# Kernel optimization log

Measured on AMD Instinct MI355X. Metric: run time of the kernel, lower is better.

## Reference

```python
import jax, jax.numpy as jnp
import numpy as np

B = 64          # batched user graphs
NPG = 512       # nodes per subgraph
N = B * NPG     # total batched nodes
DEG = 16
E = N * DEG     # edges per batched graph
DIM = 128
NUM_ENT = 1_000_000
M = 50          # candidate news entities
MASK_ID = 201659


def setup_inputs() -> dict:
    key = jax.random.key(0)
    ks = jax.random.split(key, 12)
    entity_emb = jax.random.normal(ks[0], (NUM_ENT, DIM), dtype=jnp.float32) * 0.02
    fc_w = jax.random.normal(ks[1], (DIM, DIM), dtype=jnp.float32) * 0.05
    attn_w = jax.random.normal(ks[2], (2 * DIM,), dtype=jnp.float32) * 0.05
    l_node_idx = jax.random.randint(ks[3], (N,), 0, NUM_ENT)
    s_node_idx = jax.random.randint(ks[4], (N,), 0, NUM_ENT)
    # edges confined to their own subgraph: offset by graph id
    gid = jnp.arange(E) // DEG // NPG  # [E], graph id per edge
    offs = gid * NPG
    l_src = offs + jax.random.randint(ks[5], (E,), 0, NPG)
    l_dst = offs + jax.random.randint(ks[6], (E,), 0, NPG)
    s_src = offs + jax.random.randint(ks[7], (E,), 0, NPG)
    s_dst = offs + jax.random.randint(ks[8], (E,), 0, NPG)
    goffs = jnp.arange(B) * NPG
    l_roots = goffs + jax.random.randint(ks[9], (B,), 0, NPG)
    s_roots = goffs + jax.random.randint(ks[10], (B,), 0, NPG)
    news_entities_id = jax.random.randint(ks[11], (B, M), 0, NUM_ENT)
    return {
        'entity_emb': entity_emb, 'fc_w': fc_w, 'attn_w': attn_w,
        'l_node_idx': l_node_idx, 's_node_idx': s_node_idx,
        'l_src': l_src, 'l_dst': l_dst, 's_src': s_src, 's_dst': s_dst,
        'l_roots': l_roots, 's_roots': s_roots,
        'news_entities_id': news_entities_id,
        'l_counter': 3, 's_counter': 3,
    }


def _gat(h0, src, dst, fc_w, attn_w, iters):
    """GATLayer.forward: edge attention computed once, then `iters` rounds of
    edge-softmax weighted neighbor aggregation (nodes w/o in-edges keep h)."""
    n = h0.shape[0]
    z = h0 @ fc_w  # fc (no bias)
    # e = leaky_relu(attn_fc([z_src, z_dst]))  -- [E]
    e = jax.nn.leaky_relu(z[src] @ attn_w[:DIM] + z[dst] @ attn_w[DIM:])
    # edge softmax per destination node (stable)
    m = jax.ops.segment_max(e, dst, num_segments=n)
    ex = jnp.exp(e - m[dst])
    denom = jax.ops.segment_sum(ex, dst, num_segments=n)
    alpha = ex / denom[dst]  # [E]
    has_in = jax.ops.segment_sum(jnp.ones_like(e), dst, num_segments=n) > 0
    h = z
    for _ in range(iters):
        msg = alpha[:, None] * h[src]                      # [E, DIM]
        h_new = jax.ops.segment_sum(msg, dst, num_segments=n)
        h = jnp.where(has_in[:, None], h_new, h)
    return h


def reference(entity_emb, fc_w, attn_w, l_node_idx, s_node_idx,
              l_src, l_dst, s_src, s_dst, l_roots, s_roots,
              news_entities_id, l_counter, s_counter):
    l_iters = int(l_counter) - 1
    s_iters = int(s_counter) - 1
    # long-term interest graph
    h_l = _gat(entity_emb[l_node_idx], l_src, l_dst, fc_w, attn_w, l_iters)
    l_interest = h_l[l_roots][:, None, :]   # [B,1,DIM]
    # short-term interest graph
    h_s = _gat(entity_emb[s_node_idx], s_src, s_dst, fc_w, attn_w, s_iters)
    s_interest = h_s[s_roots][:, None, :]   # [B,1,DIM]
    query = jnp.concatenate([l_interest, s_interest], axis=1)  # [B,2,DIM]
    mask = jnp.where(news_entities_id == MASK_ID, 0, news_entities_id)
    mask = mask[:, None, :].astype(jnp.float32)                # [B,1,M]
    news_emb = entity_emb[news_entities_id]                    # [B,M,DIM]
    scores = jnp.einsum('bqd,bmd->bqm', query, news_emb) / np.sqrt(DIM).astype(np.float32)
    atten = jax.nn.softmax(scores, axis=1)  # softmax over the 2 queries
    tmp = jnp.sum(scores * atten, axis=1, keepdims=True)       # [B,1,M]
    outs = jnp.sum(jnp.where(mask == 0, mask, tmp), axis=2, keepdims=True)  # [B,1,1]
    return outs
```

## Files before the change

### kernel.cpp

```cpp
#include <hip/hip_runtime.h>
#include <hip/hip_bf16.h>

#define DIM 128
#define NPG 512
#define EPG 8192
#define MAX_K 64
#define MAX_SLOTS 64
#define MASK_ID 201659

__device__ __forceinline__ float dot4(float4 a, float4 b) {
    return a.x * b.x + a.y * b.y + a.z * b.z + a.w * b.w;
}
__device__ __forceinline__ float hwred32(float p) {
    #pragma unroll
    for (int m = 16; m >= 1; m >>= 1) p += __shfl_xor(p, m);
    return p;
}
__device__ __forceinline__ float lrelu_exp(float x) {
    float lr = (x >= 0.f) ? x : 0.01f * x;
    return expf(lr);
}

__global__ __launch_bounds__(512) void k_root(
    const float* __restrict__ emb,
    const int* __restrict__ nidx_l, const int* __restrict__ nidx_s,
    const float* __restrict__ fcw, const float* __restrict__ attnw,
    const int* __restrict__ lsrc, const int* __restrict__ ldst,
    const int* __restrict__ ssrc, const int* __restrict__ sdst,
    const int* __restrict__ lroots, const int* __restrict__ sroots,
    float* __restrict__ interest)
{
    const int b = blockIdx.x, g = b >> 6, sg = b & 63, t = threadIdx.x;
    const int* src  = g ? ssrc : lsrc;
    const int* dst  = g ? sdst : ldst;
    const int* nidx = g ? nidx_s : nidx_l;
    const int root  = (g ? sroots : lroots)[sg];
    const int nbase = sg * NPG, ebase = sg * EPG;
    const int rootl = root - nbase;

    __shared__ unsigned epk[EPG];
    __shared__ float u[MAX_K][DIM];
    __shared__ short slot[MAX_K][MAX_SLOTS];
    __shared__ int   idx[NPG];
    __shared__ int   nidxs[NPG];
    __shared__ short nodeof[MAX_K];
    __shared__ int   cnt[MAX_K];
    __shared__ float wroot[MAX_SLOTS];
    __shared__ float wsrc[DIM], wdst[DIM], vvec[DIM];
    __shared__ float part[4][DIM];
    __shared__ int   Ksh;
    __shared__ float dn0sh;

    idx[t] = (t == rootl) ? 0 : -1;
    if (t < MAX_K) cnt[t] = 0;
    if (t == 0) { Ksh = 1; nodeof[0] = (short)rootl; }
    __syncthreads();

    {
        const int4* s4 = (const int4*)(src + ebase);
        const int4* d4 = (const int4*)(dst + ebase);
        #pragma unroll
        for (int i = t; i < EPG / 4; i += 512) {
            int4 s = s4[i], d = d4[i];
            unsigned p0 = ((unsigned)(s.x - nbase) << 16) | (unsigned)(d.x - nbase);
            unsigned p1 = ((unsigned)(s.y - nbase) << 16) | (unsigned)(d.y - nbase);
            unsigned p2 = ((unsigned)(s.z - nbase) << 16) | (unsigned)(d.z - nbase);
            unsigned p3 = ((unsigned)(s.w - nbase) << 16) | (unsigned)(d.w - nbase);
            ((uint4*)epk)[i] = make_uint4(p0, p1, p2, p3);
            unsigned v[4] = {p0, p1, p2, p3};
            #pragma unroll
            for (int q = 0; q < 4; q++) {
                if ((v[q] & 0xffffu) == (unsigned)rootl) {
                    int s2 = v[q] >> 16;
                    if (atomicCAS(&idx[s2], -1, -2) == -1) {
                        int k = atomicAdd(&Ksh, 1);
                        if (k < MAX_K) { nodeof[k] = (short)s2; idx[s2] = k; }
                        else idx[s2] = -1;
                    }
                }
            }
        }
        nidxs[t] = nidx[nbase + t];
        if (t < 256) {
            const float4* f4 = (const float4*)fcw;
            const float4* a4 = (const float4*)(attnw + ((t >= 128) ? DIM : 0));
            int k = t & 127;
            float s = 0.f;
            #pragma unroll 8
            for (int j = 0; j < 32; j++) s += dot4(f4[k * 32 + j], a4[j]);
            if (t < 128) wsrc[k] = s; else wdst[k] = s;
        }
    }
    __syncthreads();

    {
        const uint4* ep4 = (const uint4*)epk;
        for (int i = t; i < EPG / 4; i += 512) {
            uint4 e = ep4[i];
            unsigned v[4] = {e.x, e.y, e.z, e.w};
            #pragma unroll
            for (int q = 0; q < 4; q++) {
                int k = idx[v[q] & 0xffffu];
                if (k >= 0) {
                    int p = atomicAdd(&cnt[k], 1);
                    if (p < MAX_SLOTS) slot[k][p] = (short)(v[q] >> 16);
                }
            }
        }
    }
    __syncthreads();

    const int hwq = t >> 5, lane = t & 31;
    const int K = min(Ksh, MAX_K);
    const float4* e4 = (const float4*)emb;
    {
        float4 ws4 = ((const float4*)wsrc)[lane];
        float4 wd4 = ((const float4*)wdst)[lane];
        for (int k = hwq; k < K; k += 16) {
            int c = min(cnt[k], MAX_SLOTS);
            float4 rd = e4[(size_t)nidxs[nodeof[k]] * 32 + lane];
            float ad = hwred32(dot4(rd, wd4));
            float4 acc = make_float4(0.f, 0.f, 0.f, 0.f);
            float dn = 0.f;
            const short* sl = slot[k];
            for (int j = 0; j < c; j += 4) {
                int j1 = j + 1, j2 = j + 2, j3 = j + 3;
                bool v1 = j1 < c, v2 = j2 < c, v3 = j3 < c;
                int s0 = sl[j], s1 = sl[v1 ? j1 : j],
                    s2 = sl[v2 ? j2 : j], s3 = sl[v3 ? j3 : j];
                float4 r0 = e4[(size_t)nidxs[s0] * 32 + lane];
                float4 r1 = e4[(size_t)nidxs[s1] * 32 + lane];
                float4 r2 = e4[(size_t)nidxs[s2] * 32 + lane];
                float4 r3 = e4[(size_t)nidxs[s3] * 32 + lane];
                float p0 = hwred32(dot4(r0, ws4));
                float p1 = hwred32(dot4(r1, ws4));
                float p2 = hwred32(dot4(r2, ws4));
                float p3 = hwred32(dot4(r3, ws4));
                float w0 = lrelu_exp(p0 + ad);
                float w1 = v1 ? lrelu_exp(p1 + ad) : 0.f;
                float w2 = v2 ? lrelu_exp(p2 + ad) : 0.f;
                float w3 = v3 ? lrelu_exp(p3 + ad) : 0.f;
                dn += (w0 + w1) + (w2 + w3);
                acc.x += w0 * r0.x + w1 * r1.x + w2 * r2.x + w3 * r3.x;
                acc.y += w0 * r0.y + w1 * r1.y + w2 * r2.y + w3 * r3.y;
                acc.z += w0 * r0.z + w1 * r1.z + w2 * r2.z + w3 * r3.z;
                acc.w += w0 * r0.w + w1 * r1.w + w2 * r2.w + w3 * r3.w;
                if (k == 0 && lane == 0) {
                    wroot[j] = w0;
                    if (v1) wroot[j1] = w1;
                    if (v2) wroot[j2] = w2;
                    if (v3) wroot[j3] = w3;
                }
            }
            float4 o;
            if (c > 0) {
                float rr = 1.f / dn;
                o = make_float4(acc.x * rr, acc.y * rr, acc.z * rr, acc.w * rr);
            } else {
                o = rd;
            }
            ((float4*)u[k])[lane] = o;
            if (k == 0 && lane == 0) dn0sh = dn;
        }
    }
    __syncthreads();

    {
        int c0 = min(cnt[0], MAX_SLOTS);
        if (hwq < 4) {
            float4 acc = make_float4(0.f, 0.f, 0.f, 0.f);
            for (int j = hwq; j < c0; j += 4) {
                int s = slot[0][j];
                int ks = idx[s];
                float w = wroot[j];
                float4 uv = (ks >= 0) ? ((float4*)u[ks])[lane]
                                      : e4[(size_t)nidxs[s] * 32 + lane];
                acc.x += w * uv.x; acc.y += w * uv.y;
                acc.z += w * uv.z; acc.w += w * uv.w;
            }
            ((float4*)part[hwq])[lane] = acc;
        }
    }
    __syncthreads();
    if (hwq == 0) {
        int c0 = min(cnt[0], MAX_SLOTS);
        float4 o;
        if (c0 > 0) {
            float4 a0 = ((float4*)part[0])[lane], a1 = ((float4*)part[1])[lane];
            float4 a2 = ((float4*)part[2])[lane], a3 = ((float4*)part[3])[lane];
            float rr = 1.f / dn0sh;
            o.x = (a0.x + a1.x + a2.x + a3.x) * rr;
            o.y = (a0.y + a1.y + a2.y + a3.y) * rr;
            o.z = (a0.z + a1.z + a2.z + a3.z) * rr;
            o.w = (a0.w + a1.w + a2.w + a3.w) * rr;
        } else {
            o = ((float4*)u[0])[lane];
        }
        ((float4*)vvec)[lane] = o;
    }
    __syncthreads();

    {
        int n = t & 127, q = t >> 7;
        float s = 0.f;
        #pragma unroll 8
        for (int k2 = q * 32; k2 < q * 32 + 32; k2++) s += vvec[k2] * fcw[k2 * 128 + n];
        part[q][n] = s;
    }
    __syncthreads();
    if (t < 128) {
        float s = part[0][t] + part[1][t] + part[2][t] + part[3][t];
        interest[((size_t)g * 64 + sg) * DIM + t] = s;
    }
}

__global__ __launch_bounds__(256) void k_score(
    const float* __restrict__ emb, const int* __restrict__ news_ids,
    const float* __restrict__ interest, float* __restrict__ out)
{
    __shared__ int ids[50];
    __shared__ float ps[4];
    const int b = blockIdx.x, t = threadIdx.x;
    const int wave = t >> 6, lane = t & 63;
    if (t < 50) ids[t] = news_ids[b * 50 + t];
    __syncthreads();

    float2 q0 = ((const float2*)(interest + (size_t)b * DIM))[lane];
    float2 q1 = ((const float2*)(interest + ((size_t)64 + b) * DIM))[lane];
    const float inv_sqrtd = 0.08838834764831845f;

    float partial = 0.f;
    #pragma unroll 4
    for (int m = wave; m < 50; m += 4) {
        int id = ids[m];
        float2 nv = ((const float2*)(emb + (size_t)id * DIM))[lane];
        float p0 = q0.x * nv.x + q0.y * nv.y;
        float p1 = q1.x * nv.x + q1.y * nv.y;
        #pragma unroll
        for (int mm = 32; mm >= 1; mm >>= 1) {
            p0 += __shfl_xor(p0, mm);
            p1 += __shfl_xor(p1, mm);
        }
        float s0 = p0 * inv_sqrtd, s1 = p1 * inv_sqrtd;
        float mx = fmaxf(s0, s1);
        float e0 = expf(s0 - mx), e1 = expf(s1 - mx);
        float val = (s0 * e0 + s1 * e1) / (e0 + e1);
        partial += (id != 0 && id != MASK_ID) ? val : 0.f;
    }
    if (lane == 0) ps[wave] = partial;
    __syncthreads();
    if (t == 0) out[b] = ps[0] + ps[1] + ps[2] + ps[3];
}

extern "C" void kernel_launch(void* const* d_in, const int* in_sizes, int n_in,
                              void* d_out, int out_size, void* d_ws, size_t ws_size,
                              hipStream_t stream) {
    const float* emb   = (const float*)d_in[0];
    const float* fcw   = (const float*)d_in[1];
    const float* attnw = (const float*)d_in[2];
    const int* l_nidx  = (const int*)d_in[3];
    const int* s_nidx  = (const int*)d_in[4];
    const int* l_src   = (const int*)d_in[5];
    const int* l_dst   = (const int*)d_in[6];
    const int* s_src   = (const int*)d_in[7];
    const int* s_dst   = (const int*)d_in[8];
    const int* l_roots = (const int*)d_in[9];
    const int* s_roots = (const int*)d_in[10];
    const int* news    = (const int*)d_in[11];
    float* out = (float*)d_out;

    float* interest = (float*)d_ws;

    k_root<<<128, 512, 0, stream>>>(emb, l_nidx, s_nidx, fcw, attnw,
                                    l_src, l_dst, s_src, s_dst,
                                    l_roots, s_roots, interest);
    k_score<<<64, 256, 0, stream>>>(emb, news, interest, out);
}
```

Before: 35.66 us.

## Keep packed edges in registers and use 16-lane groups per neighbor row

The packed edge list is no longer staged in a shared-memory array. Each thread keeps its 16 packed edges in registers and reuses them for both the root-neighbor discovery pass and the slot-filling pass, which removes the LDS write and reread. The neighbor aggregation now gives each node to a 16-lane group instead of a 32-lane half-wave, with each lane handling two float4 chunks. This doubles the number of nodes processed at once and shortens the shuffle reduction, at the cost of more registers per thread.

```diff
diff --git a/kernel.cpp b/kernel.cpp
--- a/kernel.cpp
+++ b/kernel.cpp
@@ -11,9 +11,9 @@
 __device__ __forceinline__ float dot4(float4 a, float4 b) {
     return a.x * b.x + a.y * b.y + a.z * b.z + a.w * b.w;
 }
-__device__ __forceinline__ float hwred32(float p) {
+__device__ __forceinline__ float red16(float p) {
     #pragma unroll
-    for (int m = 16; m >= 1; m >>= 1) p += __shfl_xor(p, m);
+    for (int m = 8; m >= 1; m >>= 1) p += __shfl_xor(p, m);
     return p;
 }
 __device__ __forceinline__ float lrelu_exp(float x) {
@@ -38,7 +38,6 @@
     const int nbase = sg * NPG, ebase = sg * EPG;
     const int rootl = root - nbase;
 
-    __shared__ unsigned epk[EPG];
     __shared__ float u[MAX_K][DIM];
     __shared__ short slot[MAX_K][MAX_SLOTS];
     __shared__ int   idx[NPG];
@@ -56,27 +55,26 @@
     if (t == 0) { Ksh = 1; nodeof[0] = (short)rootl; }
     __syncthreads();
 
+    unsigned ep[16];
     {
         const int4* s4 = (const int4*)(src + ebase);
         const int4* d4 = (const int4*)(dst + ebase);
         #pragma unroll
-        for (int i = t; i < EPG / 4; i += 512) {
-            int4 s = s4[i], d = d4[i];
-            unsigned p0 = ((unsigned)(s.x - nbase) << 16) | (unsigned)(d.x - nbase);
-            unsigned p1 = ((unsigned)(s.y - nbase) << 16) | (unsigned)(d.y - nbase);
-            unsigned p2 = ((unsigned)(s.z - nbase) << 16) | (unsigned)(d.z - nbase);
-            unsigned p3 = ((unsigned)(s.w - nbase) << 16) | (unsigned)(d.w - nbase);
-            ((uint4*)epk)[i] = make_uint4(p0, p1, p2, p3);
-            unsigned v[4] = {p0, p1, p2, p3};
-            #pragma unroll
-            for (int q = 0; q < 4; q++) {
-                if ((v[q] & 0xffffu) == (unsigned)rootl) {
-                    int s2 = v[q] >> 16;
-                    if (atomicCAS(&idx[s2], -1, -2) == -1) {
-                        int k = atomicAdd(&Ksh, 1);
-                        if (k < MAX_K) { nodeof[k] = (short)s2; idx[s2] = k; }
-                        else idx[s2] = -1;
-                    }
+        for (int i = 0; i < 4; i++) {
+            int4 s = s4[t + 512 * i], d = d4[t + 512 * i];
+            ep[4*i+0] = ((unsigned)(s.x - nbase) << 16) | (unsigned)(d.x - nbase);
+            ep[4*i+1] = ((unsigned)(s.y - nbase) << 16) | (unsigned)(d.y - nbase);
+            ep[4*i+2] = ((unsigned)(s.z - nbase) << 16) | (unsigned)(d.z - nbase);
+            ep[4*i+3] = ((unsigned)(s.w - nbase) << 16) | (unsigned)(d.w - nbase);
+        }
+        #pragma unroll
+        for (int i = 0; i < 16; i++) {
+            if ((ep[i] & 0xffffu) == (unsigned)rootl) {
+                int s2 = ep[i] >> 16;
+                if (atomicCAS(&idx[s2], -1, -2) == -1) {
+                    int k = atomicAdd(&Ksh, 1);
+                    if (k < MAX_K) { nodeof[k] = (short)s2; idx[s2] = k; }
+                    else idx[s2] = -1;
                 }
             }
         }
@@ -93,34 +91,29 @@
     }
     __syncthreads();
 
-    {
-        const uint4* ep4 = (const uint4*)epk;
-        for (int i = t; i < EPG / 4; i += 512) {
-            uint4 e = ep4[i];
-            unsigned v[4] = {e.x, e.y, e.z, e.w};
-            #pragma unroll
-            for (int q = 0; q < 4; q++) {
-                int k = idx[v[q] & 0xffffu];
-                if (k >= 0) {
-                    int p = atomicAdd(&cnt[k], 1);
-                    if (p < MAX_SLOTS) slot[k][p] = (short)(v[q] >> 16);
-                }
-            }
-        }
-    }
-    __syncthreads();
-
-    const int hwq = t >> 5, lane = t & 31;
+    #pragma unroll
+    for (int i = 0; i < 16; i++) {
+        int k = idx[ep[i] & 0xffffu];
+        if (k >= 0) {
+            int p = atomicAdd(&cnt[k], 1);
+            if (p < MAX_SLOTS) slot[k][p] = (short)(ep[i] >> 16);
+        }
+    }
+    __syncthreads();
+
+    const int grp = t >> 4, l16 = t & 15;
     const int K = min(Ksh, MAX_K);
     const float4* e4 = (const float4*)emb;
     {
-        float4 ws4 = ((const float4*)wsrc)[lane];
-        float4 wd4 = ((const float4*)wdst)[lane];
-        for (int k = hwq; k < K; k += 16) {
+        float4 wsa = ((const float4*)wsrc)[l16], wsb = ((const float4*)wsrc)[l16 + 16];
+        float4 wda = ((const float4*)wdst)[l16], wdb = ((const float4*)wdst)[l16 + 16];
+        for (int k = grp; k < K; k += 32) {
             int c = min(cnt[k], MAX_SLOTS);
-            float4 rd = e4[(size_t)nidxs[nodeof[k]] * 32 + lane];
-            float ad = hwred32(dot4(rd, wd4));
-            float4 acc = make_float4(0.f, 0.f, 0.f, 0.f);
+            const float4* rp = e4 + (size_t)nidxs[nodeof[k]] * 32;
+            float4 rda = rp[l16], rdb = rp[l16 + 16];
+            float ad = red16(dot4(rda, wda) + dot4(rdb, wdb));
+            float4 acca = make_float4(0.f, 0.f, 0.f, 0.f);
+            float4 accb = make_float4(0.f, 0.f, 0.f, 0.f);
             float dn = 0.f;
             const short* sl = slot[k];
             for (int j = 0; j < c; j += 4) {
@@ -128,43 +121,54 @@
                 bool v1 = j1 < c, v2 = j2 < c, v3 = j3 < c;
                 int s0 = sl[j], s1 = sl[v1 ? j1 : j],
                     s2 = sl[v2 ? j2 : j], s3 = sl[v3 ? j3 : j];
-                float4 r0 = e4[(size_t)nidxs[s0] * 32 + lane];
-                float4 r1 = e4[(size_t)nidxs[s1] * 32 + lane];
-                float4 r2 = e4[(size_t)nidxs[s2] * 32 + lane];
-                float4 r3 = e4[(size_t)nidxs[s3] * 32 + lane];
-                float p0 = hwred32(dot4(r0, ws4));
-                float p1 = hwred32(dot4(r1, ws4));
-                float p2 = hwred32(dot4(r2, ws4));
-                float p3 = hwred32(dot4(r3, ws4));
+                const float4* p0r = e4 + (size_t)nidxs[s0] * 32;
+                const float4* p1r = e4 + (size_t)nidxs[s1] * 32;
+                const float4* p2r = e4 + (size_t)nidxs[s2] * 32;
+                const float4* p3r = e4 + (size_t)nidxs[s3] * 32;
+                float4 r0a = p0r[l16], r0b = p0r[l16 + 16];
+                float4 r1a = p1r[l16], r1b = p1r[l16 + 16];
+                float4 r2a = p2r[l16], r2b = p2r[l16 + 16];
+                float4 r3a = p3r[l16], r3b = p3r[l16 + 16];
+                float p0 = red16(dot4(r0a, wsa) + dot4(r0b, wsb));
+                float p1 = red16(dot4(r1a, wsa) + dot4(r1b, wsb));
+                float p2 = red16(dot4(r2a, wsa) + dot4(r2b, wsb));
+                float p3 = red16(dot4(r3a, wsa) + dot4(r3b, wsb));
                 float w0 = lrelu_exp(p0 + ad);
                 float w1 = v1 ? lrelu_exp(p1 + ad) : 0.f;
                 float w2 = v2 ? lrelu_exp(p2 + ad) : 0.f;
                 float w3 = v3 ? lrelu_exp(p3 + ad) : 0.f;
                 dn += (w0 + w1) + (w2 + w3);
-                acc.x += w0 * r0.x + w1 * r1.x + w2 * r2.x + w3 * r3.x;
-                acc.y += w0 * r0.y + w1 * r1.y + w2 * r2.y + w3 * r3.y;
-                acc.z += w0 * r0.z + w1 * r1.z + w2 * r2.z + w3 * r3.z;
-                acc.w += w0 * r0.w + w1 * r1.w + w2 * r2.w + w3 * r3.w;
-                if (k == 0 && lane == 0) {
+                acca.x += w0*r0a.x + w1*r1a.x + w2*r2a.x + w3*r3a.x;
+                acca.y += w0*r0a.y + w1*r1a.y + w2*r2a.y + w3*r3a.y;
+                acca.z += w0*r0a.z + w1*r1a.z + w2*r2a.z + w3*r3a.z;
+                acca.w += w0*r0a.w + w1*r1a.w + w2*r2a.w + w3*r3a.w;
+                accb.x += w0*r0b.x + w1*r1b.x + w2*r2b.x + w3*r3b.x;
+                accb.y += w0*r0b.y + w1*r1b.y + w2*r2b.y + w3*r3b.y;
+                accb.z += w0*r0b.z + w1*r1b.z + w2*r2b.z + w3*r3b.z;
+                accb.w += w0*r0b.w + w1*r1b.w + w2*r2b.w + w3*r3b.w;
+                if (k == 0 && l16 == 0) {
                     wroot[j] = w0;
                     if (v1) wroot[j1] = w1;
                     if (v2) wroot[j2] = w2;
                     if (v3) wroot[j3] = w3;
                 }
             }
-            float4 o;
+            float4 oa, ob;
             if (c > 0) {
                 float rr = 1.f / dn;
-                o = make_float4(acc.x * rr, acc.y * rr, acc.z * rr, acc.w * rr);
+                oa = make_float4(acca.x*rr, acca.y*rr, acca.z*rr, acca.w*rr);
+                ob = make_float4(accb.x*rr, accb.y*rr, accb.z*rr, accb.w*rr);
             } else {
-                o = rd;
-            }
-            ((float4*)u[k])[lane] = o;
-            if (k == 0 && lane == 0) dn0sh = dn;
-        }
-    }
-    __syncthreads();
-
+                oa = rda; ob = rdb;
+            }
+            ((float4*)u[k])[l16] = oa;
+            ((float4*)u[k])[l16 + 16] = ob;
+            if (k == 0 && l16 == 0) dn0sh = dn;
+        }
+    }
+    __syncthreads();
+
+    const int hwq = t >> 5, lane = t & 31;
     {
         int c0 = min(cnt[0], MAX_SLOTS);
         if (hwq < 4) {
```

Result: faster. 32.75 us, median of 2 (-8.2%).
